# Kernel optimization log

Measured on AMD Instinct MI355X. Metric: run time of the kernel, lower is better.

## Reference

```python
import jax, jax.numpy as jnp
import numpy as np

B, L, K, D_IN, UNITS, LATENT = 4, 4096, 32, 128, 128, 64


def setup_inputs() -> dict:
    key = jax.random.key(0)
    ks = jax.random.split(key, 8)
    s = 1.0 / np.sqrt(D_IN)
    return {
        "x": jax.random.normal(ks[0], (B, L, D_IN), jnp.float32),
        "position_embedding": jax.random.normal(ks[1], (B, L, K, UNITS), jnp.float32),
        "nn_idx": jax.random.randint(ks[2], (B, L, K), 0, L, jnp.int32),
        "Wq": jax.random.normal(ks[3], (D_IN, UNITS), jnp.float32) * s,
        "Wk": jax.random.normal(ks[4], (D_IN, UNITS), jnp.float32) * s,
        "Wv": jax.random.normal(ks[5], (D_IN, UNITS), jnp.float32) * s,
        "Wa0": jax.random.normal(ks[6], (UNITS, LATENT), jnp.float32) * (1.0 / np.sqrt(UNITS)),
        "Wa1": jax.random.normal(ks[7], (LATENT, UNITS), jnp.float32) * (1.0 / np.sqrt(LATENT)),
    }


def reference(x, position_embedding, nn_idx, Wq, Wk, Wv, Wa0, Wa1):
    # projections: [B,L,units]
    query = x @ Wq
    key = x @ Wk
    value = x @ Wv

    # per-batch gather of K neighbors along the length axis -> [B,L,K,units]
    gather = jax.vmap(lambda t, idx: t[idx])
    key_n = gather(key, nn_idx)
    val_n = gather(value, nn_idx)

    # relative query-key relation: [B,L,K,units]
    qk = query[:, :, None, :] - key_n

    # position-aware attention MLP: relu(Dense) -> Dense, softmax over neighbor axis K
    attn = jax.nn.relu((qk + position_embedding) @ Wa0) @ Wa1
    attn = jax.nn.softmax(attn, axis=-2)  # per-channel softmax over K

    # weighted aggregation over neighbors -> [B,L,units]
    out = jnp.sum((val_n + position_embedding) * attn, axis=-2)
    return out
```

## Files before the change

kernel.cpp:

```cpp
#include <hip/hip_runtime.h>

#define BL 16384
#define LQ 4096

typedef unsigned int uint;
typedef __attribute__((ext_vector_type(8))) short short8;
typedef __attribute__((ext_vector_type(4))) float floatx4;

union F8 { uint u[4]; uint4 u4; short8 s; };

static __device__ __forceinline__ uint f2bf(float f) {
    uint x = __float_as_uint(f);
    x += 0x7fffu + ((x >> 16) & 1u);
    return x >> 16;
}
static __device__ __forceinline__ float bf2f(uint h) { return __uint_as_float(h << 16); }
static __device__ __forceinline__ uint pk(float lo, float hi) {
    return f2bf(lo) | (f2bf(hi) << 16);
}

__global__ __launch_bounds__(256, 4) void qkv_mfma(
    const float* __restrict__ x, const float* __restrict__ Wq,
    const float* __restrict__ Wk, const float* __restrict__ Wv,
    float* __restrict__ qkvb)
{
    __shared__ uint4 wfh[4][8][64];
    __shared__ uint4 wfl[4][8][64];
    const int tid  = threadIdx.x;
    const int lane = tid & 63;
    const int w    = tid >> 6;
    const int q    = lane >> 4;
    const int c    = lane & 15;
    const int proj = blockIdx.y;
    const float* W = (proj == 0) ? Wq : (proj == 1) ? Wk : Wv;
    float* outb = qkvb + (size_t)proj * BL * 128;

    for (int e = tid; e < 32 * 64; e += 256) {
        const int f = e >> 6, ln = e & 63;
        const int ks = f >> 3, Nt = f & 7;
        const int lq = ln >> 4, lc = ln & 15;
        const float* wp = W + (ks * 32 + lq * 8) * 128 + Nt * 16 + lc;
        F8 hi, lo;
        #pragma unroll
        for (int j = 0; j < 4; ++j) {
            const float a = wp[(2 * j) * 128], b = wp[(2 * j + 1) * 128];
            const uint ha = f2bf(a), hb = f2bf(b);
            hi.u[j] = ha | (hb << 16);
            lo.u[j] = pk(a - bf2f(ha), b - bf2f(hb));
        }
        wfh[ks][Nt][ln] = hi.u4;
        wfl[ks][Nt][ln] = lo.u4;
    }
    __syncthreads();

    floatx4 acc[8];
    #pragma unroll
    for (int i = 0; i < 8; ++i) acc[i] = {0.f, 0.f, 0.f, 0.f};

    const int arow = blockIdx.x * 64 + w * 16 + c;
    #pragma unroll
    for (int ks = 0; ks < 4; ++ks) {
        const float* xp = x + arow * 128 + ks * 32 + q * 8;
        const float4 xa = ((const float4*)xp)[0];
        const float4 xb = ((const float4*)xp)[1];
        const float xv[8] = {xa.x, xa.y, xa.z, xa.w, xb.x, xb.y, xb.z, xb.w};
        F8 xh, xl;
        #pragma unroll
        for (int j = 0; j < 4; ++j) {
            const uint ha = f2bf(xv[2 * j]), hb = f2bf(xv[2 * j + 1]);
            xh.u[j] = ha | (hb << 16);
            xl.u[j] = pk(xv[2 * j] - bf2f(ha), xv[2 * j + 1] - bf2f(hb));
        }
        #pragma unroll
        for (int Nt = 0; Nt < 8; ++Nt) {
            F8 wh, wl;
            wh.u4 = wfh[ks][Nt][lane];
            wl.u4 = wfl[ks][Nt][lane];
            acc[Nt] = __builtin_amdgcn_mfma_f32_16x16x32_bf16(xh.s, wh.s, acc[Nt], 0, 0, 0);
            acc[Nt] = __builtin_amdgcn_mfma_f32_16x16x32_bf16(xh.s, wl.s, acc[Nt], 0, 0, 0);
            acc[Nt] = __builtin_amdgcn_mfma_f32_16x16x32_bf16(xl.s, wh.s, acc[Nt], 0, 0, 0);
        }
    }
    const int orow = blockIdx.x * 64 + w * 16 + q * 4;
    #pragma unroll
    for (int Nt = 0; Nt < 8; ++Nt)
        #pragma unroll
        for (int r = 0; r < 4; ++r)
            outb[(orow + r) * 128 + Nt * 16 + c] = acc[Nt][r];
}

__global__ __launch_bounds__(256, 4) void attn_mfma(
    const float* __restrict__ pos, const int* __restrict__ nn_idx,
    const float* __restrict__ qb, const float* __restrict__ kb,
    const float* __restrict__ vb, const float* __restrict__ Wa0,
    const float* __restrict__ Wa1, float* __restrict__ out)
{
    __shared__ uint4 wa0f[16][64];
    __shared__ uint4 wa1f[16][64];
    const int tid  = threadIdx.x;
    const int lane = tid & 63;
    const int w    = tid >> 6;
    const int q    = lane >> 4;
    const int c    = lane & 15;

    for (int e = tid; e < 16 * 64; e += 256) {
        const int f = e >> 6, ln = e & 63;
        const int Mt = f >> 2, ks = f & 3;
        const int lq = ln >> 4, lc = ln & 15;
        const float* wp = Wa0 + (ks * 32 + lq * 8) * 64 + Mt * 16 + lc;
        F8 v;
        #pragma unroll
        for (int j = 0; j < 4; ++j) v.u[j] = pk(wp[(2 * j) * 64], wp[(2 * j + 1) * 64]);
        wa0f[f][ln] = v.u4;
    }
    for (int e = tid; e < 16 * 64; e += 256) {
        const int f = e >> 6, ln = e & 63;
        const int ks = f >> 3, Nt = f & 7;
        const int lq = ln >> 4, lc = ln & 15;
        const float* wp = Wa1 + (ks * 32 + lq * 8) * 128 + Nt * 16 + lc;
        F8 v;
        #pragma unroll
        for (int j = 0; j < 4; ++j) v.u[j] = pk(wp[(2 * j) * 128], wp[(2 * j + 1) * 128]);
        wa1f[f][ln] = v.u4;
    }
    __syncthreads();

    const int p     = blockIdx.x * 4 + w;
    const int bbase = (p >> 12) << 12;

    const int idx0 = nn_idx[p * 32 + c];
    const int idx1 = nn_idx[p * 32 + 16 + c];
    const int r0   = (bbase + idx0) * 128;
    const int r1   = (bbase + idx1) * 128;
    const int pr0  = (p * 32 + c) * 128;
    const int pr1  = pr0 + 16 * 128;

    floatx4 acc1[4][2];
    #pragma unroll
    for (int i = 0; i < 4; ++i) { acc1[i][0] = {0.f,0.f,0.f,0.f}; acc1[i][1] = {0.f,0.f,0.f,0.f}; }

    #pragma unroll
    for (int ks = 0; ks < 4; ++ks) {
        const int u0 = ks * 32 + q * 8;
        const float4 qa = *(const float4*)(qb + p * 128 + u0);
        const float4 qc = *(const float4*)(qb + p * 128 + u0 + 4);
        F8 bfrag[2];
        #pragma unroll
        for (int Nt = 0; Nt < 2; ++Nt) {
            const int kr = (Nt == 0 ? r0 : r1) + u0;
            const int pr = (Nt == 0 ? pr0 : pr1) + u0;
            const float4 ka = *(const float4*)(kb + kr);
            const float4 kc = *(const float4*)(kb + kr + 4);
            const float4 pa = *(const float4*)(pos + pr);
            const float4 pc = *(const float4*)(pos + pr + 4);
            const float t0 = qa.x - ka.x + pa.x, t1 = qa.y - ka.y + pa.y;
            const float t2 = qa.z - ka.z + pa.z, t3 = qa.w - ka.w + pa.w;
            const float t4 = qc.x - kc.x + pc.x, t5 = qc.y - kc.y + pc.y;
            const float t6 = qc.z - kc.z + pc.z, t7 = qc.w - kc.w + pc.w;
            bfrag[Nt].u[0] = pk(t0, t1); bfrag[Nt].u[1] = pk(t2, t3);
            bfrag[Nt].u[2] = pk(t4, t5); bfrag[Nt].u[3] = pk(t6, t7);
        }
        #pragma unroll
        for (int Mt = 0; Mt < 4; ++Mt) {
            F8 a1; a1.u4 = wa0f[Mt * 4 + ks][lane];
            acc1[Mt][0] = __builtin_amdgcn_mfma_f32_16x16x32_bf16(a1.s, bfrag[0].s, acc1[Mt][0], 0, 0, 0);
            acc1[Mt][1] = __builtin_amdgcn_mfma_f32_16x16x32_bf16(a1.s, bfrag[1].s, acc1[Mt][1], 0, 0, 0);
        }
    }

    F8 a2[2][2];
    #pragma unroll
    for (int Mt2 = 0; Mt2 < 2; ++Mt2) {
        #pragma unroll
        for (int ks = 0; ks < 2; ++ks) {
            float vv[8];
            #pragma unroll
            for (int t = 0; t < 8; ++t) {
                const int sl = c + 16 * ((q & 1) * 2 + (t >> 2));
                const float vA = __shfl(acc1[2 * ks + 0][Mt2][t & 3], sl, 64);
                const float vB = __shfl(acc1[2 * ks + 1][Mt2][t & 3], sl, 64);
                vv[t] = fmaxf((q < 2) ? vA : vB, 0.f);
            }
            #pragma unroll
            for (int j = 0; j < 4; ++j) a2[Mt2][ks].u[j] = pk(vv[2 * j], vv[2 * j + 1]);
        }
    }

    int vrow[2][4], prow[2][4];
    #pragma unroll
    for (int Mt2 = 0; Mt2 < 2; ++Mt2)
        #pragma unroll
        for (int r = 0; r < 4; ++r) {
            const int knb  = Mt2 * 16 + q * 4 + r;
            const int sidx = __shfl(Mt2 == 0 ? idx0 : idx1, q * 4 + r, 64);
            vrow[Mt2][r] = (bbase + sidx) * 128;
            prow[Mt2][r] = (p * 32 + knb) * 128;
        }

    #pragma unroll
    for (int Nt2 = 0; Nt2 < 8; ++Nt2) {
        F8 b0, b1;
        b0.u4 = wa1f[Nt2][lane];
        b1.u4 = wa1f[8 + Nt2][lane];
        floatx4 a2c[2];
        a2c[0] = {0.f,0.f,0.f,0.f}; a2c[1] = {0.f,0.f,0.f,0.f};
        #pragma unroll
        for (int Mt2 = 0; Mt2 < 2; ++Mt2) {
            a2c[Mt2] = __builtin_amdgcn_mfma_f32_16x16x32_bf16(a2[Mt2][0].s, b0.s, a2c[Mt2], 0, 0, 0);
            a2c[Mt2] = __builtin_amdgcn_mfma_f32_16x16x32_bf16(a2[Mt2][1].s, b1.s, a2c[Mt2], 0, 0, 0);
        }
        const int cg = Nt2 * 16 + c;
        float se = 0.f, ov = 0.f;
        #pragma unroll
        for (int Mt2 = 0; Mt2 < 2; ++Mt2)
            #pragma unroll
            for (int r = 0; r < 4; ++r) {
                const float e  = __expf(a2c[Mt2][r]);
                const float vp = vb[vrow[Mt2][r] + cg] + pos[prow[Mt2][r] + cg];
                se += e;
                ov = fmaf(e, vp, ov);
            }
        se += __shfl_xor(se, 16, 64); ov += __shfl_xor(ov, 16, 64);
        se += __shfl_xor(se, 32, 64); ov += __shfl_xor(ov, 32, 64);
        if (q == 0) out[p * 128 + cg] = ov / se;
    }
}

extern "C" void kernel_launch(void* const* d_in, const int* in_sizes, int n_in,
                              void* d_out, int out_size, void* d_ws, size_t ws_size,
                              hipStream_t stream) {
    const float* x    = (const float*)d_in[0];
    const float* pos  = (const float*)d_in[1];
    const int*   nidx = (const int*)  d_in[2];
    const float* Wq   = (const float*)d_in[3];
    const float* Wk   = (const float*)d_in[4];
    const float* Wv   = (const float*)d_in[5];
    const float* Wa0  = (const float*)d_in[6];
    const float* Wa1  = (const float*)d_in[7];
    float* outp = (float*)d_out;

    float* qkvb = (float*)d_ws;
    const float* qbp = qkvb;
    const float* kbp = qkvb + (size_t)BL * 128;
    const float* vbp = qkvb + (size_t)2 * BL * 128;

    qkv_mfma<<<dim3(BL / 64, 3), 256, 0, stream>>>(x, Wq, Wk, Wv, qkvb);
    attn_mfma<<<BL / 4, 256, 0, stream>>>(pos, nidx, qbp, kbp, vbp, Wa0, Wa1, outp);
}
```

Measured before the change: 475.8 us.

## Persistent per-wave loop with pos prefetch and LDS-staged bf16 value+pos

Each wave now handles 8 consecutive points in a loop instead of one, so the Wa0/Wa1 fragment setup is amortized over more work. The next point's position embeddings and neighbor indices are prefetched into registers while the current point computes. Value rows are loaded with coalesced float4 reads alongside the key rows, combined with pos, and stored as bf16 in per-wave LDS. This replaces the scalar strided global gathers in the softmax aggregation. In exchange it raises register pressure (launch bounds lowered to 2), uses more LDS, cuts the grid to 512 blocks, and rounds value+pos to bf16.

After: 476.9 us. Within noise of the previous version (+0.2%).

```diff
diff --git a/kernel.cpp b/kernel.cpp
--- a/kernel.cpp
+++ b/kernel.cpp
@@ -2,8 +2,10 @@
 
 #define BL 16384
 #define LQ 4096
+#define VPS 136
 
 typedef unsigned int uint;
+typedef unsigned short ushort;
 typedef __attribute__((ext_vector_type(8))) short short8;
 typedef __attribute__((ext_vector_type(4))) float floatx4;
 
@@ -89,7 +91,7 @@
             outb[(orow + r) * 128 + Nt * 16 + c] = acc[Nt][r];
 }
 
-__global__ __launch_bounds__(256, 4) void attn_mfma(
+__global__ __launch_bounds__(256, 2) void attn_mfma(
     const float* __restrict__ pos, const int* __restrict__ nn_idx,
     const float* __restrict__ qb, const float* __restrict__ kb,
     const float* __restrict__ vb, const float* __restrict__ Wa0,
@@ -97,6 +99,8 @@
 {
     __shared__ uint4 wa0f[16][64];
     __shared__ uint4 wa1f[16][64];
+    __shared__ __attribute__((aligned(16))) ushort vpL[4][32 * VPS];
+
     const int tid  = threadIdx.x;
     const int lane = tid & 63;
     const int w    = tid >> 6;
@@ -125,104 +129,137 @@
     }
     __syncthreads();
 
-    const int p     = blockIdx.x * 4 + w;
-    const int bbase = (p >> 12) << 12;
-
-    const int idx0 = nn_idx[p * 32 + c];
-    const int idx1 = nn_idx[p * 32 + 16 + c];
-    const int r0   = (bbase + idx0) * 128;
-    const int r1   = (bbase + idx1) * 128;
-    const int pr0  = (p * 32 + c) * 128;
-    const int pr1  = pr0 + 16 * 128;
-
-    floatx4 acc1[4][2];
-    #pragma unroll
-    for (int i = 0; i < 4; ++i) { acc1[i][0] = {0.f,0.f,0.f,0.f}; acc1[i][1] = {0.f,0.f,0.f,0.f}; }
-
-    #pragma unroll
-    for (int ks = 0; ks < 4; ++ks) {
-        const int u0 = ks * 32 + q * 8;
-        const float4 qa = *(const float4*)(qb + p * 128 + u0);
-        const float4 qc = *(const float4*)(qb + p * 128 + u0 + 4);
-        F8 bfrag[2];
-        #pragma unroll
-        for (int Nt = 0; Nt < 2; ++Nt) {
-            const int kr = (Nt == 0 ? r0 : r1) + u0;
-            const int pr = (Nt == 0 ? pr0 : pr1) + u0;
-            const float4 ka = *(const float4*)(kb + kr);
-            const float4 kc = *(const float4*)(kb + kr + 4);
-            const float4 pa = *(const float4*)(pos + pr);
-            const float4 pc = *(const float4*)(pos + pr + 4);
-            const float t0 = qa.x - ka.x + pa.x, t1 = qa.y - ka.y + pa.y;
-            const float t2 = qa.z - ka.z + pa.z, t3 = qa.w - ka.w + pa.w;
-            const float t4 = qc.x - kc.x + pc.x, t5 = qc.y - kc.y + pc.y;
-            const float t6 = qc.z - kc.z + pc.z, t7 = qc.w - kc.w + pc.w;
-            bfrag[Nt].u[0] = pk(t0, t1); bfrag[Nt].u[1] = pk(t2, t3);
-            bfrag[Nt].u[2] = pk(t4, t5); bfrag[Nt].u[3] = pk(t6, t7);
-        }
-        #pragma unroll
-        for (int Mt = 0; Mt < 4; ++Mt) {
-            F8 a1; a1.u4 = wa0f[Mt * 4 + ks][lane];
-            acc1[Mt][0] = __builtin_amdgcn_mfma_f32_16x16x32_bf16(a1.s, bfrag[0].s, acc1[Mt][0], 0, 0, 0);
-            acc1[Mt][1] = __builtin_amdgcn_mfma_f32_16x16x32_bf16(a1.s, bfrag[1].s, acc1[Mt][1], 0, 0, 0);
-        }
-    }
-
-    F8 a2[2][2];
-    #pragma unroll
-    for (int Mt2 = 0; Mt2 < 2; ++Mt2) {
-        #pragma unroll
-        for (int ks = 0; ks < 2; ++ks) {
-            float vv[8];
-            #pragma unroll
-            for (int t = 0; t < 8; ++t) {
-                const int sl = c + 16 * ((q & 1) * 2 + (t >> 2));
-                const float vA = __shfl(acc1[2 * ks + 0][Mt2][t & 3], sl, 64);
-                const float vB = __shfl(acc1[2 * ks + 1][Mt2][t & 3], sl, 64);
-                vv[t] = fmaxf((q < 2) ? vA : vB, 0.f);
-            }
-            #pragma unroll
-            for (int j = 0; j < 4; ++j) a2[Mt2][ks].u[j] = pk(vv[2 * j], vv[2 * j + 1]);
-        }
-    }
-
-    int vrow[2][4], prow[2][4];
-    #pragma unroll
-    for (int Mt2 = 0; Mt2 < 2; ++Mt2)
-        #pragma unroll
-        for (int r = 0; r < 4; ++r) {
-            const int knb  = Mt2 * 16 + q * 4 + r;
-            const int sidx = __shfl(Mt2 == 0 ? idx0 : idx1, q * 4 + r, 64);
-            vrow[Mt2][r] = (bbase + sidx) * 128;
-            prow[Mt2][r] = (p * 32 + knb) * 128;
-        }
-
-    #pragma unroll
-    for (int Nt2 = 0; Nt2 < 8; ++Nt2) {
-        F8 b0, b1;
-        b0.u4 = wa1f[Nt2][lane];
-        b1.u4 = wa1f[8 + Nt2][lane];
-        floatx4 a2c[2];
-        a2c[0] = {0.f,0.f,0.f,0.f}; a2c[1] = {0.f,0.f,0.f,0.f};
+    const int pbase = (blockIdx.x * 4 + w) * 8;
+
+    float4 PF[4][2][2];
+    int pidx0, pidx1;
+    {
+        const int p = pbase;
+        pidx0 = nn_idx[p * 32 + c];
+        pidx1 = nn_idx[p * 32 + 16 + c];
+        #pragma unroll
+        for (int ks = 0; ks < 4; ++ks)
+            #pragma unroll
+            for (int Nt = 0; Nt < 2; ++Nt) {
+                const float* pp = pos + ((size_t)(p * 32 + Nt * 16 + c) * 128 + ks * 32 + q * 8);
+                PF[ks][Nt][0] = ((const float4*)pp)[0];
+                PF[ks][Nt][1] = ((const float4*)pp)[1];
+            }
+    }
+
+    for (int it = 0; it < 8; ++it) {
+        const int p     = pbase + it;
+        const int bbase = (p >> 12) << 12;
+        const int r0    = (bbase + pidx0) * 128;
+        const int r1    = (bbase + pidx1) * 128;
+
+        float4 qv[4][2];
+        #pragma unroll
+        for (int ks = 0; ks < 4; ++ks) {
+            const float* qp = qb + p * 128 + ks * 32 + q * 8;
+            qv[ks][0] = ((const float4*)qp)[0];
+            qv[ks][1] = ((const float4*)qp)[1];
+        }
+
+        floatx4 acc1[4][2];
+        #pragma unroll
+        for (int i = 0; i < 4; ++i) { acc1[i][0] = {0.f,0.f,0.f,0.f}; acc1[i][1] = {0.f,0.f,0.f,0.f}; }
+
+        #pragma unroll
+        for (int ks = 0; ks < 4; ++ks) {
+            const int u0 = ks * 32 + q * 8;
+            F8 bfrag[2];
+            #pragma unroll
+            for (int Nt = 0; Nt < 2; ++Nt) {
+                const int kr = (Nt ? r1 : r0) + u0;
+                const float4 ka = *(const float4*)(kb + kr);
+                const float4 kc = *(const float4*)(kb + kr + 4);
+                const float4 va = *(const float4*)(vb + kr);
+                const float4 vc = *(const float4*)(vb + kr + 4);
+                const float4 pa = PF[ks][Nt][0];
+                const float4 pc = PF[ks][Nt][1];
+                const float4 qa = qv[ks][0], qc = qv[ks][1];
+                const float t0 = qa.x - ka.x + pa.x, t1 = qa.y - ka.y + pa.y;
+                const float t2 = qa.z - ka.z + pa.z, t3 = qa.w - ka.w + pa.w;
+                const float t4 = qc.x - kc.x + pc.x, t5 = qc.y - kc.y + pc.y;
+                const float t6 = qc.z - kc.z + pc.z, t7 = qc.w - kc.w + pc.w;
+                bfrag[Nt].u[0] = pk(t0, t1); bfrag[Nt].u[1] = pk(t2, t3);
+                bfrag[Nt].u[2] = pk(t4, t5); bfrag[Nt].u[3] = pk(t6, t7);
+                F8 vpp;
+                vpp.u[0] = pk(va.x + pa.x, va.y + pa.y);
+                vpp.u[1] = pk(va.z + pa.z, va.w + pa.w);
+                vpp.u[2] = pk(vc.x + pc.x, vc.y + pc.y);
+                vpp.u[3] = pk(vc.z + pc.z, vc.w + pc.w);
+                *(uint4*)&vpL[w][(Nt * 16 + c) * VPS + u0] = vpp.u4;
+            }
+            #pragma unroll
+            for (int Mt = 0; Mt < 4; ++Mt) {
+                F8 a1; a1.u4 = wa0f[Mt * 4 + ks][lane];
+                acc1[Mt][0] = __builtin_amdgcn_mfma_f32_16x16x32_bf16(a1.s, bfrag[0].s, acc1[Mt][0], 0, 0, 0);
+                acc1[Mt][1] = __builtin_amdgcn_mfma_f32_16x16x32_bf16(a1.s, bfrag[1].s, acc1[Mt][1], 0, 0, 0);
+            }
+        }
+
+        {
+            const int pn = (p + 1 < BL) ? (p + 1) : p;
+            pidx0 = nn_idx[pn * 32 + c];
+            pidx1 = nn_idx[pn * 32 + 16 + c];
+            #pragma unroll
+            for (int ks = 0; ks < 4; ++ks)
+                #pragma unroll
+                for (int Nt = 0; Nt < 2; ++Nt) {
+                    const float* pp = pos + ((size_t)(pn * 32 + Nt * 16 + c) * 128 + ks * 32 + q * 8);
+                    PF[ks][Nt][0] = ((const float4*)pp)[0];
+                    PF[ks][Nt][1] = ((const float4*)pp)[1];
+                }
+        }
+
+        F8 a2[2][2];
         #pragma unroll
         for (int Mt2 = 0; Mt2 < 2; ++Mt2) {
-            a2c[Mt2] = __builtin_amdgcn_mfma_f32_16x16x32_bf16(a2[Mt2][0].s, b0.s, a2c[Mt2], 0, 0, 0);
-            a2c[Mt2] = __builtin_amdgcn_mfma_f32_16x16x32_bf16(a2[Mt2][1].s, b1.s, a2c[Mt2], 0, 0, 0);
-        }
-        const int cg = Nt2 * 16 + c;
-        float se = 0.f, ov = 0.f;
-        #pragma unroll
-        for (int Mt2 = 0; Mt2 < 2; ++Mt2)
-            #pragma unroll
-            for (int r = 0; r < 4; ++r) {
-                const float e  = __expf(a2c[Mt2][r]);
-                const float vp = vb[vrow[Mt2][r] + cg] + pos[prow[Mt2][r] + cg];
-                se += e;
-                ov = fmaf(e, vp, ov);
-            }
-        se += __shfl_xor(se, 16, 64); ov += __shfl_xor(ov, 16, 64);
-        se += __shfl_xor(se, 32, 64); ov += __shfl_xor(ov, 32, 64);
-        if (q == 0) out[p * 128 + cg] = ov / se;
+            #pragma unroll
+            for (int ks = 0; ks < 2; ++ks) {
+                float vv[8];
+                #pragma unroll
+                for (int t = 0; t < 8; ++t) {
+                    const int sl = c + 16 * ((q & 1) * 2 + (t >> 2));
+                    const float vA = __shfl(acc1[2 * ks + 0][Mt2][t & 3], sl, 64);
+                    const float vB = __shfl(acc1[2 * ks + 1][Mt2][t & 3], sl, 64);
+                    vv[t] = fmaxf((q < 2) ? vA : vB, 0.f);
+                }
+                #pragma unroll
+                for (int j = 0; j < 4; ++j) a2[Mt2][ks].u[j] = pk(vv[2 * j], vv[2 * j + 1]);
+            }
+        }
+
+        #pragma unroll
+        for (int Nt2 = 0; Nt2 < 8; ++Nt2) {
+            F8 b0, b1;
+            b0.u4 = wa1f[Nt2][lane];
+            b1.u4 = wa1f[8 + Nt2][lane];
+            floatx4 a2c[2];
+            a2c[0] = {0.f,0.f,0.f,0.f}; a2c[1] = {0.f,0.f,0.f,0.f};
+            #pragma unroll
+            for (int Mt2 = 0; Mt2 < 2; ++Mt2) {
+                a2c[Mt2] = __builtin_amdgcn_mfma_f32_16x16x32_bf16(a2[Mt2][0].s, b0.s, a2c[Mt2], 0, 0, 0);
+                a2c[Mt2] = __builtin_amdgcn_mfma_f32_16x16x32_bf16(a2[Mt2][1].s, b1.s, a2c[Mt2], 0, 0, 0);
+            }
+            const int cg = Nt2 * 16 + c;
+            float se = 0.f, ov = 0.f;
+            #pragma unroll
+            for (int Mt2 = 0; Mt2 < 2; ++Mt2)
+                #pragma unroll
+                for (int r = 0; r < 4; ++r) {
+                    const int   kk = Mt2 * 16 + q * 4 + r;
+                    const float e  = __expf(a2c[Mt2][r]);
+                    const float vp = bf2f(vpL[w][kk * VPS + cg]);
+                    se += e;
+                    ov = fmaf(e, vp, ov);
+                }
+            se += __shfl_xor(se, 16, 64); ov += __shfl_xor(ov, 16, 64);
+            se += __shfl_xor(se, 32, 64); ov += __shfl_xor(ov, 32, 64);
+            if (q == 0) out[p * 128 + cg] = ov / se;
+        }
     }
 }
 
@@ -245,5 +282,5 @@
     const float* vbp = qkvb + (size_t)2 * BL * 128;
 
     qkv_mfma<<<dim3(BL / 64, 3), 256, 0, stream>>>(x, Wq, Wk, Wv, qkvb);
-    attn_mfma<<<BL / 4, 256, 0, stream>>>(pos, nidx, qbp, kbp, vbp, Wa0, Wa1, outp);
-}
+    attn_mfma<<<BL / 8 / 4, 256, 0, stream>>>(pos, nidx, qbp, kbp, vbp, Wa0, Wa1, outp);
+}
```
